# Optimization experiments

Hardware: AMD Instinct MI355X
Metric: run time of the kernel (lower is better)

## Reference

```python
import jax, jax.numpy as jnp
import numpy as np

N = 10000        # num nodes
E = 160000       # num edges
C = 128          # hidden_channels
SCALE = 0.0625   # scale_factor = 1/avg_degree
EPS = 1.1920929e-07  # torch RMSNorm default eps = finfo(float32).eps


def setup_inputs() -> dict:
    key = jax.random.key(0)
    ks = jax.random.split(key, 10)
    s = jax.random.normal(ks[0], (N, 1, C), dtype=jnp.float32)
    v = jax.random.normal(ks[1], (N, 3, C), dtype=jnp.float32)
    edge_index = jax.random.randint(ks[2], (2, E), 0, N, dtype=jnp.int64)
    rbf_filter = jax.random.normal(ks[3], (E, 1, 3 * C), dtype=jnp.float32)
    edge_vector = jax.random.normal(ks[4], (E, 3), dtype=jnp.float32)
    # phi MLP params (Linear(C,C) -> SiLU -> Dropout(eval) -> Linear(C,3C))
    w1 = jax.random.normal(ks[5], (C, C), dtype=jnp.float32) / np.sqrt(C)
    b1 = jnp.zeros((C,), dtype=jnp.float32)
    w2 = jax.random.normal(ks[6], (3 * C, C), dtype=jnp.float32) / np.sqrt(C)
    b2 = jnp.zeros((3 * C,), dtype=jnp.float32)
    rms_w = jnp.ones((C,), dtype=jnp.float32)  # RMSNorm elementwise affine weight
    return {"s": s, "v": v, "edge_index": edge_index, "rbf_filter": rbf_filter,
            "edge_vector": edge_vector, "w1": w1, "b1": b1, "w2": w2, "b2": b2,
            "rms_w": rms_w}


def reference(s, v, edge_index, rbf_filter, edge_vector, w1, b1, w2, b2, rms_w):
    i, j = edge_index[0], edge_index[1]
    # RMSNorm over last dim
    s_norm = s * jax.lax.rsqrt(jnp.mean(s * s, axis=-1, keepdims=True) + EPS) * rms_w
    # phi MLP (dropout is identity in eval mode)
    h = jax.nn.silu(jnp.einsum('nkc,dc->nkd', s_norm, w1) + b1)
    phi_s = jnp.einsum('nkc,dc->nkd', h, w2) + b2          # [N,1,3C]
    filt = phi_s[j] * rbf_filter                           # [E,1,3C]
    m_s, m_vv, m_vs = jnp.split(filt, 3, axis=-1)          # each [E,1,C]
    ds = jax.ops.segment_sum(m_s, i, num_segments=N)       # [N,1,C]
    gate = v[j] * m_vv + edge_vector[:, :, None] * m_vs    # [E,3,C]
    dv = jax.ops.segment_sum(gate, i, num_segments=N)      # [N,3,C]
    s_out = s + ds * SCALE
    v_out = v + dv * SCALE
    return s_out, v_out
```

## Files before the change

kernel.cpp:

```cpp
#include <hip/hip_runtime.h>
#include <math.h>

#define NN 10000
#define NE 160000
#define CH 128
#define SCALE_F 0.0625f
#define EPS_F 1.1920929e-07f

__device__ __forceinline__ unsigned short f2bf(float x) {
    unsigned int u = __float_as_uint(x);
    u += 0x7FFFu + ((u >> 16) & 1u);
    return (unsigned short)(u >> 16);
}
__device__ __forceinline__ unsigned int pack2bf(float a, float b) {
    return (unsigned int)f2bf(a) | ((unsigned int)f2bf(b) << 16);
}
__device__ __forceinline__ float bf_lo(unsigned int u) { return __uint_as_float(u << 16); }
__device__ __forceinline__ float bf_hi(unsigned int u) { return __uint_as_float(u & 0xFFFF0000u); }

__global__ __launch_bounds__(256) void detect_zero_kernel(const int* __restrict__ ei,
                                                          int* __restrict__ flag,
                                                          int* __restrict__ counts) {
    int t = blockIdx.x * 256 + threadIdx.x;
    if (t < NN) counts[t] = 0;
    if (blockIdx.x == 0 && threadIdx.x < 64) {
        int val = ei[2 * threadIdx.x + 1];
        unsigned long long b = __ballot(val != 0);
        if (threadIdx.x == 0) *flag = (b == 0ULL) ? 1 : 0;
    }
}

__global__ __launch_bounds__(256) void count_kernel(const int* __restrict__ ei,
                                                    const int* __restrict__ flag,
                                                    int* __restrict__ counts) {
    int e = blockIdx.x * 256 + threadIdx.x;
    if (e >= NE) return;
    int i = (*flag) ? ei[2 * (size_t)e] : ei[e];
    atomicAdd(&counts[i], 1);
}

__global__ __launch_bounds__(1024) void scan_kernel(const int* __restrict__ counts,
                                                    int* __restrict__ offsets,
                                                    int* __restrict__ cursor) {
    __shared__ int sm[1024];
    const int t = threadIdx.x;
    const int base = t * 10;
    int vals[10];
    int lsum = 0;
    #pragma unroll
    for (int k = 0; k < 10; ++k) {
        int idx = base + k;
        int v = (idx < NN) ? counts[idx] : 0;
        vals[k] = v;
        lsum += v;
    }
    sm[t] = lsum;
    __syncthreads();
    #pragma unroll
    for (int off = 1; off < 1024; off <<= 1) {
        int add = (t >= off) ? sm[t - off] : 0;
        __syncthreads();
        sm[t] += add;
        __syncthreads();
    }
    int run = sm[t] - lsum;
    #pragma unroll
    for (int k = 0; k < 10; ++k) {
        int idx = base + k;
        if (idx < NN) { offsets[idx] = run; cursor[idx] = run; }
        run += vals[k];
    }
}

__global__ __launch_bounds__(256) void bucket_kernel(const int* __restrict__ ei,
                                                     const int* __restrict__ flag,
                                                     int* __restrict__ cursor,
                                                     int2* __restrict__ bucket) {
    int e = blockIdx.x * 256 + threadIdx.x;
    if (e >= NE) return;
    int i, j;
    if (*flag) {
        i = ei[2 * (size_t)e];
        j = ei[2 * ((size_t)NE + e)];
    } else {
        i = ei[e];
        j = ei[NE + e];
    }
    int pos = atomicAdd(&cursor[i], 1);
    bucket[pos] = make_int2(e, j);
}

__global__ __launch_bounds__(256) void phi_kernel(const float* __restrict__ s,
                                                  const float* __restrict__ v,
                                                  const float* __restrict__ w1,
                                                  const float* __restrict__ b1,
                                                  const float* __restrict__ w2,
                                                  const float* __restrict__ b2,
                                                  const float* __restrict__ rms_w,
                                                  unsigned int* __restrict__ rec) {
    __shared__ float sn[8][132];
    __shared__ float hh[8][132];

    const int t = threadIdx.x;
    const int n0 = blockIdx.x * 8;

    {
        const int m = t >> 5;
        const int l = t & 31;
        const int n = n0 + m;
        const float2* vsrc = (const float2*)(v + (size_t)n * 384);
        unsigned int* vdst = rec + (size_t)n * 384 + 192;
        #pragma unroll
        for (int k = 0; k < 6; ++k) {
            float2 a = vsrc[k * 32 + l];
            vdst[k * 32 + l] = pack2bf(a.x, a.y);
        }
    }

    {
        const int m = t >> 5;
        const int l = t & 31;
        const int n = n0 + m;
        float4 sv = ((const float4*)(s + (size_t)n * CH))[l];
        float ss = sv.x * sv.x + sv.y * sv.y + sv.z * sv.z + sv.w * sv.w;
        #pragma unroll
        for (int off = 16; off > 0; off >>= 1) ss += __shfl_xor(ss, off, 32);
        const float sc = rsqrtf(ss * (1.0f / CH) + EPS_F);
        float4 rw = ((const float4*)rms_w)[l];
        float4* dst = (float4*)&sn[m][l * 4];
        float4 o;
        o.x = sv.x * sc * rw.x;
        o.y = sv.y * sc * rw.y;
        o.z = sv.z * sc * rw.z;
        o.w = sv.w * sc * rw.w;
        *dst = o;
    }
    __syncthreads();

    const int d  = t & 127;
    const int mh = (t >> 7) * 4;

    {
        float acc0, acc1, acc2, acc3;
        const float bb = b1[d];
        acc0 = acc1 = acc2 = acc3 = bb;
        const float4* w1v = (const float4*)(w1 + (size_t)d * CH);
        #pragma unroll 4
        for (int kc = 0; kc < 32; ++kc) {
            float4 w = w1v[kc];
            float4 s0 = *(const float4*)&sn[mh + 0][kc * 4];
            float4 s1 = *(const float4*)&sn[mh + 1][kc * 4];
            float4 s2 = *(const float4*)&sn[mh + 2][kc * 4];
            float4 s3 = *(const float4*)&sn[mh + 3][kc * 4];
            acc0 += w.x * s0.x + w.y * s0.y + w.z * s0.z + w.w * s0.w;
            acc1 += w.x * s1.x + w.y * s1.y + w.z * s1.z + w.w * s1.w;
            acc2 += w.x * s2.x + w.y * s2.y + w.z * s2.z + w.w * s2.w;
            acc3 += w.x * s3.x + w.y * s3.y + w.z * s3.z + w.w * s3.w;
        }
        hh[mh + 0][d] = acc0 / (1.0f + __expf(-acc0));
        hh[mh + 1][d] = acc1 / (1.0f + __expf(-acc1));
        hh[mh + 2][d] = acc2 / (1.0f + __expf(-acc2));
        hh[mh + 3][d] = acc3 / (1.0f + __expf(-acc3));
    }
    __syncthreads();

    {
        float a[3][4];
        #pragma unroll
        for (int q = 0; q < 3; ++q) {
            float bb = b2[q * 128 + d];
            a[q][0] = a[q][1] = a[q][2] = a[q][3] = bb;
        }
        const float4* w2v0 = (const float4*)(w2 + (size_t)(0 * 128 + d) * CH);
        const float4* w2v1 = (const float4*)(w2 + (size_t)(1 * 128 + d) * CH);
        const float4* w2v2 = (const float4*)(w2 + (size_t)(2 * 128 + d) * CH);
        #pragma unroll 2
        for (int kc = 0; kc < 32; ++kc) {
            float4 h0 = *(const float4*)&hh[mh + 0][kc * 4];
            float4 h1 = *(const float4*)&hh[mh + 1][kc * 4];
            float4 h2 = *(const float4*)&hh[mh + 2][kc * 4];
            float4 h3 = *(const float4*)&hh[mh + 3][kc * 4];
            float4 w0 = w2v0[kc];
            float4 w1r = w2v1[kc];
            float4 w2r = w2v2[kc];
            a[0][0] += w0.x * h0.x + w0.y * h0.y + w0.z * h0.z + w0.w * h0.w;
            a[0][1] += w0.x * h1.x + w0.y * h1.y + w0.z * h1.z + w0.w * h1.w;
            a[0][2] += w0.x * h2.x + w0.y * h2.y + w0.z * h2.z + w0.w * h2.w;
            a[0][3] += w0.x * h3.x + w0.y * h3.y + w0.z * h3.z + w0.w * h3.w;
            a[1][0] += w1r.x * h0.x + w1r.y * h0.y + w1r.z * h0.z + w1r.w * h0.w;
            a[1][1] += w1r.x * h1.x + w1r.y * h1.y + w1r.z * h1.z + w1r.w * h1.w;
            a[1][2] += w1r.x * h2.x + w1r.y * h2.y + w1r.z * h2.z + w1r.w * h2.w;
            a[1][3] += w1r.x * h3.x + w1r.y * h3.y + w1r.z * h3.z + w1r.w * h3.w;
            a[2][0] += w2r.x * h0.x + w2r.y * h0.y + w2r.z * h0.z + w2r.w * h0.w;
            a[2][1] += w2r.x * h1.x + w2r.y * h1.y + w2r.z * h1.z + w2r.w * h1.w;
            a[2][2] += w2r.x * h2.x + w2r.y * h2.y + w2r.z * h2.z + w2r.w * h2.w;
            a[2][3] += w2r.x * h3.x + w2r.y * h3.y + w2r.z * h3.z + w2r.w * h3.w;
        }
        #pragma unroll
        for (int mm = 0; mm < 4; ++mm) {
            unsigned short* p = (unsigned short*)(rec + (size_t)(n0 + mh + mm) * 384);
            p[0 * 128 + d] = f2bf(a[0][mm]);
            p[1 * 128 + d] = f2bf(a[1][mm]);
            p[2 * 128 + d] = f2bf(a[2][mm]);
        }
    }
}

__global__ __launch_bounds__(256) void gather_kernel(const float* __restrict__ s,
                                                     const float* __restrict__ v,
                                                     const unsigned int* __restrict__ rec,
                                                     const float* __restrict__ rbf,
                                                     const float* __restrict__ ev,
                                                     const int* __restrict__ offsets,
                                                     const int* __restrict__ counts,
                                                     const int2* __restrict__ bucket,
                                                     float* __restrict__ out_s,
                                                     float* __restrict__ out_v) {
    const int t = threadIdx.x;
    const int n = blockIdx.x * 4 + (t >> 6);
    const int l = t & 63;

    float2 acc_s = make_float2(0.f, 0.f);
    float2 av0 = make_float2(0.f, 0.f);
    float2 av1 = make_float2(0.f, 0.f);
    float2 av2 = make_float2(0.f, 0.f);

    const int beg = offsets[n];
    const int end = beg + counts[n];

    for (int k = beg; k < end; ++k) {
        const int2 ej = bucket[k];
        const int e = ej.x, j = ej.y;

        const unsigned int* rj = rec + (size_t)j * 384;
        const float2* rb = (const float2*)(rbf + (size_t)e * 384);

        unsigned int u_s  = rj[l];
        unsigned int u_vv = rj[64 + l];
        unsigned int u_vs = rj[128 + l];
        unsigned int u_v0 = rj[192 + l];
        unsigned int u_v1 = rj[256 + l];
        unsigned int u_v2 = rj[320 + l];

        float2 rs  = rb[l];
        float2 rvv = rb[64 + l];
        float2 rvs = rb[128 + l];

        const float e0 = ev[(size_t)e * 3 + 0];
        const float e1 = ev[(size_t)e * 3 + 1];
        const float e2 = ev[(size_t)e * 3 + 2];

        acc_s.x += bf_lo(u_s) * rs.x;
        acc_s.y += bf_hi(u_s) * rs.y;

        const float mvv_x = bf_lo(u_vv) * rvv.x;
        const float mvv_y = bf_hi(u_vv) * rvv.y;
        const float mvs_x = bf_lo(u_vs) * rvs.x;
        const float mvs_y = bf_hi(u_vs) * rvs.y;

        av0.x += bf_lo(u_v0) * mvv_x + e0 * mvs_x;
        av0.y += bf_hi(u_v0) * mvv_y + e0 * mvs_y;
        av1.x += bf_lo(u_v1) * mvv_x + e1 * mvs_x;
        av1.y += bf_hi(u_v1) * mvv_y + e1 * mvs_y;
        av2.x += bf_lo(u_v2) * mvv_x + e2 * mvs_x;
        av2.y += bf_hi(u_v2) * mvv_y + e2 * mvs_y;
    }

    {
        float2 sv = ((const float2*)(s + (size_t)n * CH))[l];
        ((float2*)(out_s + (size_t)n * CH))[l] =
            make_float2(sv.x + SCALE_F * acc_s.x, sv.y + SCALE_F * acc_s.y);

        const float2* vn = (const float2*)(v + (size_t)n * 384);
        float2 w0 = vn[l], w1 = vn[64 + l], w2 = vn[128 + l];
        float2* ov = (float2*)(out_v + (size_t)n * 384);
        ov[l]       = make_float2(w0.x + SCALE_F * av0.x, w0.y + SCALE_F * av0.y);
        ov[64 + l]  = make_float2(w1.x + SCALE_F * av1.x, w1.y + SCALE_F * av1.y);
        ov[128 + l] = make_float2(w2.x + SCALE_F * av2.x, w2.y + SCALE_F * av2.y);
    }
}

extern "C" void kernel_launch(void* const* d_in, const int* in_sizes, int n_in,
                              void* d_out, int out_size, void* d_ws, size_t ws_size,
                              hipStream_t stream) {
    const float* s    = (const float*)d_in[0];
    const float* v    = (const float*)d_in[1];
    const int*   ei   = (const int*)d_in[2];
    const float* rbf  = (const float*)d_in[3];
    const float* ev   = (const float*)d_in[4];
    const float* w1   = (const float*)d_in[5];
    const float* b1   = (const float*)d_in[6];
    const float* w2   = (const float*)d_in[7];
    const float* b2   = (const float*)d_in[8];
    const float* rmsw = (const float*)d_in[9];

    float* out   = (float*)d_out;
    float* out_s = out;
    float* out_v = out + (size_t)NN * CH;

    char* ws = (char*)d_ws;
    unsigned int* rec = (unsigned int*)ws;     ws += (size_t)NN * 384 * sizeof(unsigned int);
    int* i64flag = (int*)ws;                   ws += 64;
    int* counts  = (int*)ws;                   ws += (size_t)NN * sizeof(int);
    int* offsets = (int*)ws;                   ws += (size_t)NN * sizeof(int);
    int* cursor  = (int*)ws;                   ws += (size_t)NN * sizeof(int);
    int2* bucket = (int2*)ws;

    detect_zero_kernel<<<(NN + 255) / 256, 256, 0, stream>>>(ei, i64flag, counts);
    count_kernel<<<(NE + 255) / 256, 256, 0, stream>>>(ei, i64flag, counts);
    scan_kernel<<<1, 1024, 0, stream>>>(counts, offsets, cursor);
    bucket_kernel<<<(NE + 255) / 256, 256, 0, stream>>>(ei, i64flag, cursor, bucket);
    phi_kernel<<<NN / 8, 256, 0, stream>>>(s, v, w1, b1, w2, b2, rmsw, rec);
    gather_kernel<<<NN / 4, 256, 0, stream>>>(s, v, rec, rbf, ev, offsets, counts, bucket,
                                              out_s, out_v);
}
```

Measured before the change: 504.8 us.

## Process two edges per wavefront in gather with wider loads and packed edge vectors

The gather kernel now splits each 64-lane wavefront into two halves that each handle a different edge. Each lane covers four channels with uint2/float4 loads, and the two halves combine their partial sums with a cross-half shuffle at the end. The edge vector is converted to fp16 and packed into a wider int4 bucket entry in bucket_kernel, so the gather no longer reads it scattered from the ev array. The next bucket entry is prefetched one iteration ahead. In exchange the bucket record doubles in size, edge vectors lose precision to fp16, and odd-degree nodes need a tail path where half the lanes sit idle.

```diff
diff --git a/kernel.cpp b/kernel.cpp
--- a/kernel.cpp
+++ b/kernel.cpp
@@ -1,4 +1,5 @@
 #include <hip/hip_runtime.h>
+#include <hip/hip_fp16.h>
 #include <math.h>
 
 #define NN 10000
@@ -17,6 +18,9 @@
 }
 __device__ __forceinline__ float bf_lo(unsigned int u) { return __uint_as_float(u << 16); }
 __device__ __forceinline__ float bf_hi(unsigned int u) { return __uint_as_float(u & 0xFFFF0000u); }
+__device__ __forceinline__ float4 bfq(uint2 u) {
+    return make_float4(bf_lo(u.x), bf_hi(u.x), bf_lo(u.y), bf_hi(u.y));
+}
 
 __global__ __launch_bounds__(256) void detect_zero_kernel(const int* __restrict__ ei,
                                                           int* __restrict__ flag,
@@ -74,8 +78,9 @@
 
 __global__ __launch_bounds__(256) void bucket_kernel(const int* __restrict__ ei,
                                                      const int* __restrict__ flag,
+                                                     const float* __restrict__ ev,
                                                      int* __restrict__ cursor,
-                                                     int2* __restrict__ bucket) {
+                                                     int4* __restrict__ bucket) {
     int e = blockIdx.x * 256 + threadIdx.x;
     if (e >= NE) return;
     int i, j;
@@ -86,8 +91,15 @@
         i = ei[e];
         j = ei[NE + e];
     }
+    float e0 = ev[(size_t)e * 3 + 0];
+    float e1 = ev[(size_t)e * 3 + 1];
+    float e2 = ev[(size_t)e * 3 + 2];
+    __half2 h01 = __floats2half2_rn(e0, e1);
+    __half  h2v = __float2half_rn(e2);
+    unsigned int u01 = *reinterpret_cast<unsigned int*>(&h01);
+    unsigned int u2  = (unsigned int)(*reinterpret_cast<unsigned short*>(&h2v));
     int pos = atomicAdd(&cursor[i], 1);
-    bucket[pos] = make_int2(e, j);
+    bucket[pos] = make_int4(e, j, (int)u01, (int)u2);
 }
 
 __global__ __launch_bounds__(256) void phi_kernel(const float* __restrict__ s,
@@ -210,73 +222,160 @@
                                                      const float* __restrict__ v,
                                                      const unsigned int* __restrict__ rec,
                                                      const float* __restrict__ rbf,
-                                                     const float* __restrict__ ev,
                                                      const int* __restrict__ offsets,
                                                      const int* __restrict__ counts,
-                                                     const int2* __restrict__ bucket,
+                                                     const int4* __restrict__ bucket,
                                                      float* __restrict__ out_s,
                                                      float* __restrict__ out_v) {
     const int t = threadIdx.x;
     const int n = blockIdx.x * 4 + (t >> 6);
     const int l = t & 63;
-
-    float2 acc_s = make_float2(0.f, 0.f);
-    float2 av0 = make_float2(0.f, 0.f);
-    float2 av1 = make_float2(0.f, 0.f);
-    float2 av2 = make_float2(0.f, 0.f);
+    const int half = l >> 5;
+    const int q = l & 31;
+
+    float4 acc_s = make_float4(0.f, 0.f, 0.f, 0.f);
+    float4 av0 = acc_s, av1 = acc_s, av2 = acc_s;
 
     const int beg = offsets[n];
-    const int end = beg + counts[n];
-
-    for (int k = beg; k < end; ++k) {
-        const int2 ej = bucket[k];
-        const int e = ej.x, j = ej.y;
-
-        const unsigned int* rj = rec + (size_t)j * 384;
-        const float2* rb = (const float2*)(rbf + (size_t)e * 384);
-
-        unsigned int u_s  = rj[l];
-        unsigned int u_vv = rj[64 + l];
-        unsigned int u_vs = rj[128 + l];
-        unsigned int u_v0 = rj[192 + l];
-        unsigned int u_v1 = rj[256 + l];
-        unsigned int u_v2 = rj[320 + l];
-
-        float2 rs  = rb[l];
-        float2 rvv = rb[64 + l];
-        float2 rvs = rb[128 + l];
-
-        const float e0 = ev[(size_t)e * 3 + 0];
-        const float e1 = ev[(size_t)e * 3 + 1];
-        const float e2 = ev[(size_t)e * 3 + 2];
-
-        acc_s.x += bf_lo(u_s) * rs.x;
-        acc_s.y += bf_hi(u_s) * rs.y;
-
-        const float mvv_x = bf_lo(u_vv) * rvv.x;
-        const float mvv_y = bf_hi(u_vv) * rvv.y;
-        const float mvs_x = bf_lo(u_vs) * rvs.x;
-        const float mvs_y = bf_hi(u_vs) * rvs.y;
-
-        av0.x += bf_lo(u_v0) * mvv_x + e0 * mvs_x;
-        av0.y += bf_hi(u_v0) * mvv_y + e0 * mvs_y;
-        av1.x += bf_lo(u_v1) * mvv_x + e1 * mvs_x;
-        av1.y += bf_hi(u_v1) * mvv_y + e1 * mvs_y;
-        av2.x += bf_lo(u_v2) * mvv_x + e2 * mvs_x;
-        av2.y += bf_hi(u_v2) * mvv_y + e2 * mvs_y;
-    }
-
-    {
-        float2 sv = ((const float2*)(s + (size_t)n * CH))[l];
-        ((float2*)(out_s + (size_t)n * CH))[l] =
-            make_float2(sv.x + SCALE_F * acc_s.x, sv.y + SCALE_F * acc_s.y);
-
-        const float2* vn = (const float2*)(v + (size_t)n * 384);
-        float2 w0 = vn[l], w1 = vn[64 + l], w2 = vn[128 + l];
-        float2* ov = (float2*)(out_v + (size_t)n * 384);
-        ov[l]       = make_float2(w0.x + SCALE_F * av0.x, w0.y + SCALE_F * av0.y);
-        ov[64 + l]  = make_float2(w1.x + SCALE_F * av1.x, w1.y + SCALE_F * av1.y);
-        ov[128 + l] = make_float2(w2.x + SCALE_F * av2.x, w2.y + SCALE_F * av2.y);
+    const int deg = counts[n];
+    const int npair = deg >> 1;
+    const int4* bk = bucket + beg;
+
+    int4 ent = make_int4(0, 0, 0, 0);
+    if (npair > 0) ent = bk[half];
+
+    for (int p = 0; p < npair; ++p) {
+        int4 entn = ent;
+        if (p + 1 < npair) entn = bk[2 * (p + 1) + half];
+
+        const unsigned int* rj = rec + (size_t)ent.y * 384;
+        const float*        rb = rbf + (size_t)ent.x * 384;
+
+        uint2 uS  = ((const uint2*)(rj +   0))[q];
+        uint2 uVV = ((const uint2*)(rj +  64))[q];
+        uint2 uVS = ((const uint2*)(rj + 128))[q];
+        uint2 uV0 = ((const uint2*)(rj + 192))[q];
+        uint2 uV1 = ((const uint2*)(rj + 256))[q];
+        uint2 uV2 = ((const uint2*)(rj + 320))[q];
+        float4 rS  = ((const float4*)(rb +   0))[q];
+        float4 rVV = ((const float4*)(rb + 128))[q];
+        float4 rVS = ((const float4*)(rb + 256))[q];
+
+        __half2 h01 = *reinterpret_cast<const __half2*>(&ent.z);
+        float2 ev01 = __half22float2(h01);
+        unsigned short h2u = (unsigned short)(ent.w & 0xFFFF);
+        float ev2 = __half2float(*reinterpret_cast<const __half*>(&h2u));
+
+        float4 ps = bfq(uS);
+        acc_s.x = fmaf(ps.x, rS.x, acc_s.x);
+        acc_s.y = fmaf(ps.y, rS.y, acc_s.y);
+        acc_s.z = fmaf(ps.z, rS.z, acc_s.z);
+        acc_s.w = fmaf(ps.w, rS.w, acc_s.w);
+
+        float4 pv = bfq(uVV);
+        float4 pw = bfq(uVS);
+        float4 mvv = make_float4(pv.x * rVV.x, pv.y * rVV.y, pv.z * rVV.z, pv.w * rVV.w);
+        float4 mvs = make_float4(pw.x * rVS.x, pw.y * rVS.y, pw.z * rVS.z, pw.w * rVS.w);
+
+        float4 v0 = bfq(uV0), v1 = bfq(uV1), v2 = bfq(uV2);
+        av0.x = fmaf(v0.x, mvv.x, fmaf(ev01.x, mvs.x, av0.x));
+        av0.y = fmaf(v0.y, mvv.y, fmaf(ev01.x, mvs.y, av0.y));
+        av0.z = fmaf(v0.z, mvv.z, fmaf(ev01.x, mvs.z, av0.z));
+        av0.w = fmaf(v0.w, mvv.w, fmaf(ev01.x, mvs.w, av0.w));
+        av1.x = fmaf(v1.x, mvv.x, fmaf(ev01.y, mvs.x, av1.x));
+        av1.y = fmaf(v1.y, mvv.y, fmaf(ev01.y, mvs.y, av1.y));
+        av1.z = fmaf(v1.z, mvv.z, fmaf(ev01.y, mvs.z, av1.z));
+        av1.w = fmaf(v1.w, mvv.w, fmaf(ev01.y, mvs.w, av1.w));
+        av2.x = fmaf(v2.x, mvv.x, fmaf(ev2, mvs.x, av2.x));
+        av2.y = fmaf(v2.y, mvv.y, fmaf(ev2, mvs.y, av2.y));
+        av2.z = fmaf(v2.z, mvv.z, fmaf(ev2, mvs.z, av2.z));
+        av2.w = fmaf(v2.w, mvv.w, fmaf(ev2, mvs.w, av2.w));
+
+        ent = entn;
+    }
+
+    if ((deg & 1) && half == 0) {
+        int4 te = bk[deg - 1];
+        const unsigned int* rj = rec + (size_t)te.y * 384;
+        const float*        rb = rbf + (size_t)te.x * 384;
+
+        uint2 uS  = ((const uint2*)(rj +   0))[q];
+        uint2 uVV = ((const uint2*)(rj +  64))[q];
+        uint2 uVS = ((const uint2*)(rj + 128))[q];
+        uint2 uV0 = ((const uint2*)(rj + 192))[q];
+        uint2 uV1 = ((const uint2*)(rj + 256))[q];
+        uint2 uV2 = ((const uint2*)(rj + 320))[q];
+        float4 rS  = ((const float4*)(rb +   0))[q];
+        float4 rVV = ((const float4*)(rb + 128))[q];
+        float4 rVS = ((const float4*)(rb + 256))[q];
+
+        __half2 h01 = *reinterpret_cast<const __half2*>(&te.z);
+        float2 ev01 = __half22float2(h01);
+        unsigned short h2u = (unsigned short)(te.w & 0xFFFF);
+        float ev2 = __half2float(*reinterpret_cast<const __half*>(&h2u));
+
+        float4 ps = bfq(uS);
+        acc_s.x = fmaf(ps.x, rS.x, acc_s.x);
+        acc_s.y = fmaf(ps.y, rS.y, acc_s.y);
+        acc_s.z = fmaf(ps.z, rS.z, acc_s.z);
+        acc_s.w = fmaf(ps.w, rS.w, acc_s.w);
+
+        float4 pv = bfq(uVV);
+        float4 pw = bfq(uVS);
+        float4 mvv = make_float4(pv.x * rVV.x, pv.y * rVV.y, pv.z * rVV.z, pv.w * rVV.w);
+        float4 mvs = make_float4(pw.x * rVS.x, pw.y * rVS.y, pw.z * rVS.z, pw.w * rVS.w);
+
+        float4 v0 = bfq(uV0), v1 = bfq(uV1), v2 = bfq(uV2);
+        av0.x = fmaf(v0.x, mvv.x, fmaf(ev01.x, mvs.x, av0.x));
+        av0.y = fmaf(v0.y, mvv.y, fmaf(ev01.x, mvs.y, av0.y));
+        av0.z = fmaf(v0.z, mvv.z, fmaf(ev01.x, mvs.z, av0.z));
+        av0.w = fmaf(v0.w, mvv.w, fmaf(ev01.x, mvs.w, av0.w));
+        av1.x = fmaf(v1.x, mvv.x, fmaf(ev01.y, mvs.x, av1.x));
+        av1.y = fmaf(v1.y, mvv.y, fmaf(ev01.y, mvs.y, av1.y));
+        av1.z = fmaf(v1.z, mvv.z, fmaf(ev01.y, mvs.z, av1.z));
+        av1.w = fmaf(v1.w, mvv.w, fmaf(ev01.y, mvs.w, av1.w));
+        av2.x = fmaf(v2.x, mvv.x, fmaf(ev2, mvs.x, av2.x));
+        av2.y = fmaf(v2.y, mvv.y, fmaf(ev2, mvs.y, av2.y));
+        av2.z = fmaf(v2.z, mvv.z, fmaf(ev2, mvs.z, av2.z));
+        av2.w = fmaf(v2.w, mvv.w, fmaf(ev2, mvs.w, av2.w));
+    }
+
+    acc_s.x += __shfl_xor(acc_s.x, 32);
+    acc_s.y += __shfl_xor(acc_s.y, 32);
+    acc_s.z += __shfl_xor(acc_s.z, 32);
+    acc_s.w += __shfl_xor(acc_s.w, 32);
+    av0.x += __shfl_xor(av0.x, 32);
+    av0.y += __shfl_xor(av0.y, 32);
+    av0.z += __shfl_xor(av0.z, 32);
+    av0.w += __shfl_xor(av0.w, 32);
+    av1.x += __shfl_xor(av1.x, 32);
+    av1.y += __shfl_xor(av1.y, 32);
+    av1.z += __shfl_xor(av1.z, 32);
+    av1.w += __shfl_xor(av1.w, 32);
+    av2.x += __shfl_xor(av2.x, 32);
+    av2.y += __shfl_xor(av2.y, 32);
+    av2.z += __shfl_xor(av2.z, 32);
+    av2.w += __shfl_xor(av2.w, 32);
+
+    const size_t nb = (size_t)n;
+    if (half == 0) {
+        float4 sv = ((const float4*)(s + nb * CH))[q];
+        ((float4*)(out_s + nb * CH))[q] =
+            make_float4(sv.x + SCALE_F * acc_s.x, sv.y + SCALE_F * acc_s.y,
+                        sv.z + SCALE_F * acc_s.z, sv.w + SCALE_F * acc_s.w);
+        float4 w0 = ((const float4*)(v + nb * 384))[q];
+        ((float4*)(out_v + nb * 384))[q] =
+            make_float4(w0.x + SCALE_F * av0.x, w0.y + SCALE_F * av0.y,
+                        w0.z + SCALE_F * av0.z, w0.w + SCALE_F * av0.w);
+    } else {
+        float4 w1 = ((const float4*)(v + nb * 384 + 128))[q];
+        ((float4*)(out_v + nb * 384 + 128))[q] =
+            make_float4(w1.x + SCALE_F * av1.x, w1.y + SCALE_F * av1.y,
+                        w1.z + SCALE_F * av1.z, w1.w + SCALE_F * av1.w);
+        float4 w2 = ((const float4*)(v + nb * 384 + 256))[q];
+        ((float4*)(out_v + nb * 384 + 256))[q] =
+            make_float4(w2.x + SCALE_F * av2.x, w2.y + SCALE_F * av2.y,
+                        w2.z + SCALE_F * av2.z, w2.w + SCALE_F * av2.w);
     }
 }
 
@@ -304,13 +403,13 @@
     int* counts  = (int*)ws;                   ws += (size_t)NN * sizeof(int);
     int* offsets = (int*)ws;                   ws += (size_t)NN * sizeof(int);
     int* cursor  = (int*)ws;                   ws += (size_t)NN * sizeof(int);
-    int2* bucket = (int2*)ws;
+    int4* bucket = (int4*)ws;
 
     detect_zero_kernel<<<(NN + 255) / 256, 256, 0, stream>>>(ei, i64flag, counts);
     count_kernel<<<(NE + 255) / 256, 256, 0, stream>>>(ei, i64flag, counts);
     scan_kernel<<<1, 1024, 0, stream>>>(counts, offsets, cursor);
-    bucket_kernel<<<(NE + 255) / 256, 256, 0, stream>>>(ei, i64flag, cursor, bucket);
+    bucket_kernel<<<(NE + 255) / 256, 256, 0, stream>>>(ei, i64flag, ev, cursor, bucket);
     phi_kernel<<<NN / 8, 256, 0, stream>>>(s, v, w1, b1, w2, b2, rmsw, rec);
-    gather_kernel<<<NN / 4, 256, 0, stream>>>(s, v, rec, rbf, ev, offsets, counts, bucket,
+    gather_kernel<<<NN / 4, 256, 0, stream>>>(s, v, rec, rbf, offsets, counts, bucket,
                                               out_s, out_v);
 }
```

Result: no change. 495.9 us (-1.8%).
